# Optimization experiments

Hardware: AMD Instinct MI355X
Metric: run time of the kernel (lower is better)

The kernel has to match this reference:

```python
import jax, jax.numpy as jnp
import numpy as np

VOCAB = 100000
EMBED = 64
HIDDEN = 256
SEQ = 200
BATCH = 4096


def setup_inputs() -> dict:
    key = jax.random.key(0)
    ks = jax.random.split(key, 12)
    s = 0.02
    return {
        "user_hist": jax.random.randint(ks[0], (BATCH, SEQ), 0, VOCAB),
        "target_item": jax.random.randint(ks[1], (BATCH,), 0, VOCAB),
        "user_emb": jax.random.normal(ks[2], (VOCAB, EMBED), jnp.float32) * s,
        "item_emb": jax.random.normal(ks[3], (VOCAB, EMBED), jnp.float32) * s,
        "attn_w1": jax.random.normal(ks[4], (4 * EMBED, HIDDEN), jnp.float32) * s,
        "attn_b1": jnp.zeros((HIDDEN,), jnp.float32),
        "attn_w2": jax.random.normal(ks[5], (HIDDEN, 1), jnp.float32) * s,
        "attn_b2": jnp.zeros((1,), jnp.float32),
        "mlp_w1": jax.random.normal(ks[6], (2 * EMBED, HIDDEN), jnp.float32) * s,
        "mlp_b1": jnp.zeros((HIDDEN,), jnp.float32),
        "mlp_w2": jax.random.normal(ks[7], (HIDDEN, 1), jnp.float32) * s,
        "mlp_b2": jnp.zeros((1,), jnp.float32),
    }


def reference(user_hist, target_item, user_emb, item_emb,
              attn_w1, attn_b1, attn_w2, attn_b2,
              mlp_w1, mlp_b1, mlp_w2, mlp_b2):
    # [B, S, E] history embeddings, [B, 1, E] target embedding
    h = user_emb[user_hist]
    t = item_emb[target_item][:, None, :]
    tb = jnp.broadcast_to(t, h.shape)
    # attention MLP over [B, S, 4E]
    att_in = jnp.concatenate([h, tb, h - t, h * t], axis=-1)
    att_h = jax.nn.relu(att_in @ attn_w1 + attn_b1)
    att_logits = (att_h @ attn_w2 + attn_b2)[..., 0]            # [B, S]
    att_w = jax.nn.softmax(att_logits, axis=-1)[..., None]      # [B, S, 1]
    user_interest = jnp.sum(h * att_w, axis=1)                  # [B, E]
    # prediction head on [B, 2E]
    mlp_in = jnp.concatenate([user_interest, t[:, 0, :]], axis=-1)
    mlp_h = jax.nn.relu(mlp_in @ mlp_w1 + mlp_b1)
    out = jax.nn.sigmoid(mlp_h @ mlp_w2 + mlp_b2)               # [B, 1]
    return out
```

## Files before the change

### kernel.cpp

```cpp
#include <hip/hip_runtime.h>
#include <math.h>

#define EMBED   64
#define HIDDEN  256
#define SEQ     200
#define SEQP    208
#define MT      13

typedef _Float16 f16x8  __attribute__((ext_vector_type(8)));
typedef _Float16 half2_t __attribute__((ext_vector_type(2)));
typedef float    f32x4  __attribute__((ext_vector_type(4)));
typedef float    f32x2  __attribute__((ext_vector_type(2)));

__device__ inline float fdot2(half2_t a, half2_t b, float c) {
  return __builtin_amdgcn_fdot2(a, b, c, false);
}

__global__ void din_precompute(const float* __restrict__ attn_w1,
                               const float* __restrict__ mlp_w1,
                               uint2* __restrict__ fragB8,
                               _Float16* __restrict__ fragW3,
                               _Float16* __restrict__ D2f,
                               _Float16* __restrict__ fragB2) {
  const int gid = blockIdx.x * 256 + threadIdx.x;
  if (gid < 2048) {
    const int i = gid >> 7, rem = gid & 127, kc = rem >> 6, lane = rem & 63;
    const int n = i * 16 + (lane & 15);
    const int kb = kc * 32 + (lane >> 4) * 8;
    float v[8];
    #pragma unroll
    for (int j = 0; j < 8; ++j)
      v[j] = 16.0f * (attn_w1[(kb + j) * HIDDEN + n] + attn_w1[(128 + kb + j) * HIDDEN + n]);
    int lo = __builtin_amdgcn_cvt_pk_fp8_f32(v[0], v[1], 0, false);
    lo     = __builtin_amdgcn_cvt_pk_fp8_f32(v[2], v[3], lo, true);
    int hi = __builtin_amdgcn_cvt_pk_fp8_f32(v[4], v[5], 0, false);
    hi     = __builtin_amdgcn_cvt_pk_fp8_f32(v[6], v[7], hi, true);
    fragB8[gid] = uint2{(unsigned)lo, (unsigned)hi};
  } else if (gid < 4096) {
    const int g = gid - 2048;
    const int i = g >> 7, rem = g & 127, kc = rem >> 6, lane = rem & 63;
    const int n = i * 16 + (lane & 15);
    const int kb = kc * 32 + (lane >> 4) * 8;
    #pragma unroll
    for (int j = 0; j < 8; ++j)
      fragW3[g * 8 + j] = (_Float16)(16.0f * attn_w1[(192 + kb + j) * HIDDEN + n]);
  } else if (gid < 8192) {
    const int f = (gid - 4096) * 4;
    #pragma unroll
    for (int i = 0; i < 4; ++i) {
      const int idx = f + i;
      const int kk = idx & 7, t2 = idx >> 3;
      const int j = t2 & 255, c = t2 >> 8;
      const int k = c * 8 + kk;
      D2f[idx] = (_Float16)(attn_w1[(64 + k) * HIDDEN + j] - attn_w1[(128 + k) * HIDDEN + j]);
    }
  } else {
    const int g = gid - 8192;
    const int nt = g >> 8, kc = (g >> 6) & 3, lane = g & 63;
    const int n = nt * 16 + (lane & 15);
    const int kb = kc * 32 + (lane >> 4) * 8;
    #pragma unroll
    for (int j = 0; j < 8; ++j)
      fragB2[g * 8 + j] = (_Float16)mlp_w1[(kb + j) * HIDDEN + n];
  }
}

__global__ __launch_bounds__(512, 8)
void din_fused_kernel(const int* __restrict__ user_hist,
                      const int* __restrict__ target_item,
                      const float* __restrict__ user_emb,
                      const float* __restrict__ item_emb,
                      const float* __restrict__ attn_b1,
                      const float* __restrict__ attn_w2,
                      const float* __restrict__ mlp_b1,
                      const float* __restrict__ mlp_w2,
                      const float* __restrict__ mlp_b2,
                      const uint2* __restrict__ fragB8,
                      const _Float16* __restrict__ fragW3,
                      const _Float16* __restrict__ D2f,
                      const _Float16* __restrict__ fragB2,
                      float* __restrict__ out)
{
  __shared__ __align__(16) uint2 Hf8[MT * 2 * 64];
  __shared__ __align__(16) _Float16 t16[EMBED];
  __shared__ float cl[HIDDEN];
  __shared__ float lp[8][SEQP];
  __shared__ float weights[SEQP];
  __shared__ __align__(16) _Float16 mi16[EMBED];
  __shared__ float red[16];

  const int b    = blockIdx.x;
  const int tid  = threadIdx.x;
  const int lane = tid & 63;
  const int wave = tid >> 6;
  const int m    = lane & 15;
  const int quad = lane >> 4;

  if (tid < EMBED) t16[tid] = (_Float16)item_emb[target_item[b] * EMBED + tid];

  long long Aw8[2][2];
  #pragma unroll
  for (int i = 0; i < 2; ++i)
    #pragma unroll
    for (int c = 0; c < 2; ++c)
      Aw8[i][c] = __builtin_bit_cast(long long, fragB8[((2 * wave + i) * 2 + c) * 64 + lane]);

  {
    const int* hist = user_hist + b * SEQ;
    for (int slot = tid; slot < MT * 2 * 64; slot += 512) {
      const int ln = slot & 63, kcomb = slot >> 6;
      const int st = kcomb >> 1, kc = kcomb & 1;
      const int s = st * 16 + (ln & 15);
      const int kb = kc * 32 + (ln >> 4) * 8;
      uint2 pv = uint2{0u, 0u};
      if (s < SEQ) {
        const float4* src = reinterpret_cast<const float4*>(&user_emb[hist[s] * EMBED + kb]);
        const float4 x = src[0], y = src[1];
        int lo = __builtin_amdgcn_cvt_pk_fp8_f32(16.f * x.x, 16.f * x.y, 0, false);
        lo     = __builtin_amdgcn_cvt_pk_fp8_f32(16.f * x.z, 16.f * x.w, lo, true);
        int hi = __builtin_amdgcn_cvt_pk_fp8_f32(16.f * y.x, 16.f * y.y, 0, false);
        hi     = __builtin_amdgcn_cvt_pk_fp8_f32(16.f * y.z, 16.f * y.w, hi, true);
        pv = uint2{(unsigned)lo, (unsigned)hi};
      }
      Hf8[slot] = pv;
    }
  }
  __syncthreads();

  if (tid < HIDDEN) {
    float cj = attn_b1[tid];
    const f16x8* dp = reinterpret_cast<const f16x8*>(D2f);
    #pragma unroll
    for (int c = 0; c < 8; ++c) {
      const f16x8 dv = dp[c * HIDDEN + tid];
      const f16x8 tv = *reinterpret_cast<const f16x8*>(&t16[c * 8]);
      const half2_t* d2 = reinterpret_cast<const half2_t*>(&dv);
      const half2_t* t2 = reinterpret_cast<const half2_t*>(&tv);
      cj = fdot2(d2[0], t2[0], cj);
      cj = fdot2(d2[1], t2[1], cj);
      cj = fdot2(d2[2], t2[2], cj);
      cj = fdot2(d2[3], t2[3], cj);
    }
    cl[tid] = cj;
  }

  long long AwT[2][2];
  #pragma unroll
  for (int i = 0; i < 2; ++i)
    #pragma unroll
    for (int c = 0; c < 2; ++c) {
      const f16x8 w3v = reinterpret_cast<const f16x8*>(fragW3)[((2 * wave + i) * 2 + c) * 64 + lane];
      const f16x8 tw  = *reinterpret_cast<const f16x8*>(&t16[c * 32 + quad * 8]);
      const f16x8 p = w3v * tw;
      int lo = __builtin_amdgcn_cvt_pk_fp8_f32((float)p[0], (float)p[1], 0, false);
      lo     = __builtin_amdgcn_cvt_pk_fp8_f32((float)p[2], (float)p[3], lo, true);
      int hi = __builtin_amdgcn_cvt_pk_fp8_f32((float)p[4], (float)p[5], 0, false);
      hi     = __builtin_amdgcn_cvt_pk_fp8_f32((float)p[6], (float)p[7], hi, true);
      AwT[i][c] = __builtin_bit_cast(long long, uint2{(unsigned)lo, (unsigned)hi});
    }
  __syncthreads();

  float cn[2][4], w2n[2][4];
  #pragma unroll
  for (int i = 0; i < 2; ++i)
    #pragma unroll
    for (int r = 0; r < 4; ++r) {
      const int n = (2 * wave + i) * 16 + quad * 4 + r;
      cn[i][r]  = 256.0f * cl[n];
      w2n[i][r] = attn_w2[n] * (1.0f / 256.0f);
    }

  for (int st = 0; st < MT; ++st) {
    const long long b0 = __builtin_bit_cast(long long, Hf8[(st * 2 + 0) * 64 + lane]);
    const long long b1 = __builtin_bit_cast(long long, Hf8[(st * 2 + 1) * 64 + lane]);
    float lg = 0.f;
    #pragma unroll
    for (int i = 0; i < 2; ++i) {
      f32x4 acc = {cn[i][0], cn[i][1], cn[i][2], cn[i][3]};
      acc = __builtin_amdgcn_mfma_f32_16x16x32_fp8_fp8(Aw8[i][0], b0, acc, 0, 0, 0);
      acc = __builtin_amdgcn_mfma_f32_16x16x32_fp8_fp8(Aw8[i][1], b1, acc, 0, 0, 0);
      acc = __builtin_amdgcn_mfma_f32_16x16x32_fp8_fp8(AwT[i][0], b0, acc, 0, 0, 0);
      acc = __builtin_amdgcn_mfma_f32_16x16x32_fp8_fp8(AwT[i][1], b1, acc, 0, 0, 0);
      #pragma unroll
      for (int r = 0; r < 4; ++r)
        lg += fmaxf(acc[r], 0.0f) * w2n[i][r];
    }
    lg += __shfl_xor(lg, 16, 64);
    lg += __shfl_xor(lg, 32, 64);
    if (lane < 16) lp[wave][st * 16 + lane] = lg;
  }
  __syncthreads();

  float v = -INFINITY;
  if (tid < SEQ)
    v = lp[0][tid] + lp[1][tid] + lp[2][tid] + lp[3][tid]
      + lp[4][tid] + lp[5][tid] + lp[6][tid] + lp[7][tid];
  float mx = v;
  #pragma unroll
  for (int off = 32; off; off >>= 1) mx = fmaxf(mx, __shfl_xor(mx, off, 64));
  if (lane == 0) red[wave] = mx;
  __syncthreads();
  mx = fmaxf(fmaxf(fmaxf(red[0], red[1]), fmaxf(red[2], red[3])),
             fmaxf(fmaxf(red[4], red[5]), fmaxf(red[6], red[7])));
  float e = (tid < SEQ) ? expf(v - mx) : 0.0f;
  float ssum = e;
  #pragma unroll
  for (int off = 32; off; off >>= 1) ssum += __shfl_xor(ssum, off, 64);
  if (lane == 0) red[8 + wave] = ssum;
  __syncthreads();
  const float tot = red[8] + red[9] + red[10] + red[11]
                  + red[12] + red[13] + red[14] + red[15];
  if (tid < SEQP) weights[tid] = (tid < SEQ) ? e / tot : 0.0f;
  __syncthreads();

  {
    const int kc = wave & 1, g = wave >> 1;
    float pk[8];
    #pragma unroll
    for (int j = 0; j < 8; ++j) pk[j] = 0.f;
    for (int st = g; st < MT; st += 4) {
      const float wt = weights[st * 16 + m];
      const uint2 hv = Hf8[(st * 2 + kc) * 64 + lane];
      const f32x2 f0 = __builtin_amdgcn_cvt_pk_f32_fp8((int)hv.x, false);
      const f32x2 f1 = __builtin_amdgcn_cvt_pk_f32_fp8((int)hv.x, true);
      const f32x2 f2 = __builtin_amdgcn_cvt_pk_f32_fp8((int)hv.y, false);
      const f32x2 f3 = __builtin_amdgcn_cvt_pk_f32_fp8((int)hv.y, true);
      pk[0] += wt * f0.x;  pk[1] += wt * f0.y;
      pk[2] += wt * f1.x;  pk[3] += wt * f1.y;
      pk[4] += wt * f2.x;  pk[5] += wt * f2.y;
      pk[6] += wt * f3.x;  pk[7] += wt * f3.y;
    }
    #pragma unroll
    for (int j = 0; j < 8; ++j) {
      float p = pk[j];
      p += __shfl_xor(p, 1, 64);
      p += __shfl_xor(p, 2, 64);
      p += __shfl_xor(p, 4, 64);
      p += __shfl_xor(p, 8, 64);
      pk[j] = p;
    }
    if (m == 0) {
      #pragma unroll
      for (int j = 0; j < 8; ++j)
        lp[g][kc * 32 + quad * 8 + j] = pk[j];
    }
  }
  __syncthreads();
  if (tid < EMBED)
    mi16[tid] = (_Float16)((lp[0][tid] + lp[1][tid] + lp[2][tid] + lp[3][tid]) * 0.0625f);
  __syncthreads();

  {
    const f16x8 mb0 = *reinterpret_cast<const f16x8*>(&mi16[quad * 8]);
    const f16x8 mb1 = *reinterpret_cast<const f16x8*>(&mi16[32 + quad * 8]);
    const f16x8 tv0 = *reinterpret_cast<const f16x8*>(&t16[quad * 8]);
    const f16x8 tv1 = *reinterpret_cast<const f16x8*>(&t16[32 + quad * 8]);
    float z = 0.f;
    #pragma unroll
    for (int i = 0; i < 2; ++i) {
      const f16x8* B2 = reinterpret_cast<const f16x8*>(fragB2) + ((2 * wave + i) * 4) * 64 + lane;
      float bb[4], ww[4];
      #pragma unroll
      for (int r = 0; r < 4; ++r) {
        const int n = (2 * wave + i) * 16 + quad * 4 + r;
        bb[r] = mlp_b1[n];
        ww[r] = mlp_w2[n];
      }
      f32x4 acc = {bb[0], bb[1], bb[2], bb[3]};
      acc = __builtin_amdgcn_mfma_f32_16x16x32_f16(B2[0],       mb0, acc, 0, 0, 0);
      acc = __builtin_amdgcn_mfma_f32_16x16x32_f16(B2[64],      mb1, acc, 0, 0, 0);
      acc = __builtin_amdgcn_mfma_f32_16x16x32_f16(B2[128],     tv0, acc, 0, 0, 0);
      acc = __builtin_amdgcn_mfma_f32_16x16x32_f16(B2[192],     tv1, acc, 0, 0, 0);
      #pragma unroll
      for (int r = 0; r < 4; ++r)
        z += fmaxf(acc[r], 0.0f) * ww[r];
    }
    z += __shfl_xor(z, 16, 64);
    z += __shfl_xor(z, 32, 64);
    if (lane == 0) red[wave] = z;
  }
  __syncthreads();
  if (tid == 0) {
    const float zz = red[0] + red[1] + red[2] + red[3]
                   + red[4] + red[5] + red[6] + red[7] + mlp_b2[0];
    out[b] = 1.0f / (1.0f + expf(-zz));
  }
}

extern "C" void kernel_launch(void* const* d_in, const int* in_sizes, int n_in,
                              void* d_out, int out_size, void* d_ws, size_t ws_size,
                              hipStream_t stream) {
  const int*   user_hist   = (const int*)  d_in[0];
  const int*   target_item = (const int*)  d_in[1];
  const float* user_emb    = (const float*)d_in[2];
  const float* item_emb    = (const float*)d_in[3];
  const float* attn_w1     = (const float*)d_in[4];
  const float* attn_b1     = (const float*)d_in[5];
  const float* attn_w2     = (const float*)d_in[6];
  const float* mlp_w1      = (const float*)d_in[8];
  const float* mlp_b1      = (const float*)d_in[9];
  const float* mlp_w2      = (const float*)d_in[10];
  const float* mlp_b2      = (const float*)d_in[11];
  float* out = (float*)d_out;

  uint2*    fragB8 = (uint2*)d_ws;
  _Float16* fragW3 = (_Float16*)((char*)d_ws + 16384);
  _Float16* D2f    = (_Float16*)((char*)d_ws + 49152);
  _Float16* fragB2 = (_Float16*)((char*)d_ws + 81920);

  din_precompute<<<48, 256, 0, stream>>>(attn_w1, mlp_w1, fragB8, fragW3, D2f, fragB2);

  const int batch = in_sizes[1];
  din_fused_kernel<<<batch, 512, 0, stream>>>(
      user_hist, target_item, user_emb, item_emb,
      attn_b1, attn_w2, mlp_b1, mlp_w2, mlp_b2,
      fragB8, fragW3, D2f, fragB2, out);
}
```

Before: 183.1 us.

## Compute per-hidden bias term with MFMA and trim softmax to four waves

Replaces the scalar fdot2 loop that built the target-dependent bias vector cl in shared memory with a per-wave f16 MFMA over MFMA-fragment-layout weights, dropping the cl buffer and one barrier. History indices are staged in shared memory before the gather, the softmax reduction runs only on the four waves that cover the sequence, and the weighted-sum loop is fully unrolled, with vectorized bias and weight loads. This reduces serial per-block prologue work and synchronization, but adds an extra barrier before the gather and changes the precompute layout.

New measurement: 180.3 us. About the same (-1.5%).

```diff
diff --git a/kernel.cpp b/kernel.cpp
--- a/kernel.cpp
+++ b/kernel.cpp
@@ -8,19 +8,14 @@
 #define MT      13
 
 typedef _Float16 f16x8  __attribute__((ext_vector_type(8)));
-typedef _Float16 half2_t __attribute__((ext_vector_type(2)));
 typedef float    f32x4  __attribute__((ext_vector_type(4)));
 typedef float    f32x2  __attribute__((ext_vector_type(2)));
-
-__device__ inline float fdot2(half2_t a, half2_t b, float c) {
-  return __builtin_amdgcn_fdot2(a, b, c, false);
-}
 
 __global__ void din_precompute(const float* __restrict__ attn_w1,
                                const float* __restrict__ mlp_w1,
                                uint2* __restrict__ fragB8,
                                _Float16* __restrict__ fragW3,
-                               _Float16* __restrict__ D2f,
+                               _Float16* __restrict__ fragDt,
                                _Float16* __restrict__ fragB2) {
   const int gid = blockIdx.x * 256 + threadIdx.x;
   if (gid < 2048) {
@@ -44,18 +39,17 @@
     #pragma unroll
     for (int j = 0; j < 8; ++j)
       fragW3[g * 8 + j] = (_Float16)(16.0f * attn_w1[(192 + kb + j) * HIDDEN + n]);
-  } else if (gid < 8192) {
-    const int f = (gid - 4096) * 4;
-    #pragma unroll
-    for (int i = 0; i < 4; ++i) {
-      const int idx = f + i;
-      const int kk = idx & 7, t2 = idx >> 3;
-      const int j = t2 & 255, c = t2 >> 8;
-      const int k = c * 8 + kk;
-      D2f[idx] = (_Float16)(attn_w1[(64 + k) * HIDDEN + j] - attn_w1[(128 + k) * HIDDEN + j]);
-    }
+  } else if (gid < 6144) {
+    const int g = gid - 4096;
+    const int i = g >> 7, rem = g & 127, kc = rem >> 6, lane = rem & 63;
+    const int n = i * 16 + (lane & 15);
+    const int kb = kc * 32 + (lane >> 4) * 8;
+    #pragma unroll
+    for (int j = 0; j < 8; ++j)
+      fragDt[g * 8 + j] = (_Float16)(attn_w1[(64 + kb + j) * HIDDEN + n]
+                                   - attn_w1[(128 + kb + j) * HIDDEN + n]);
   } else {
-    const int g = gid - 8192;
+    const int g = gid - 6144;
     const int nt = g >> 8, kc = (g >> 6) & 3, lane = g & 63;
     const int n = nt * 16 + (lane & 15);
     const int kb = kc * 32 + (lane >> 4) * 8;
@@ -77,13 +71,13 @@
                       const float* __restrict__ mlp_b2,
                       const uint2* __restrict__ fragB8,
                       const _Float16* __restrict__ fragW3,
-                      const _Float16* __restrict__ D2f,
+                      const _Float16* __restrict__ fragDt,
                       const _Float16* __restrict__ fragB2,
                       float* __restrict__ out)
 {
   __shared__ __align__(16) uint2 Hf8[MT * 2 * 64];
   __shared__ __align__(16) _Float16 t16[EMBED];
-  __shared__ float cl[HIDDEN];
+  __shared__ int   histL[SEQP];
   __shared__ float lp[8][SEQP];
   __shared__ float weights[SEQP];
   __shared__ __align__(16) _Float16 mi16[EMBED];
@@ -97,6 +91,7 @@
   const int quad = lane >> 4;
 
   if (tid < EMBED) t16[tid] = (_Float16)item_emb[target_item[b] * EMBED + tid];
+  if (tid < SEQP) histL[tid] = (tid < SEQ) ? user_hist[b * SEQ + tid] : 0;
 
   long long Aw8[2][2];
   #pragma unroll
@@ -104,72 +99,68 @@
     #pragma unroll
     for (int c = 0; c < 2; ++c)
       Aw8[i][c] = __builtin_bit_cast(long long, fragB8[((2 * wave + i) * 2 + c) * 64 + lane]);
-
-  {
-    const int* hist = user_hist + b * SEQ;
-    for (int slot = tid; slot < MT * 2 * 64; slot += 512) {
-      const int ln = slot & 63, kcomb = slot >> 6;
-      const int st = kcomb >> 1, kc = kcomb & 1;
-      const int s = st * 16 + (ln & 15);
-      const int kb = kc * 32 + (ln >> 4) * 8;
-      uint2 pv = uint2{0u, 0u};
-      if (s < SEQ) {
-        const float4* src = reinterpret_cast<const float4*>(&user_emb[hist[s] * EMBED + kb]);
-        const float4 x = src[0], y = src[1];
-        int lo = __builtin_amdgcn_cvt_pk_fp8_f32(16.f * x.x, 16.f * x.y, 0, false);
-        lo     = __builtin_amdgcn_cvt_pk_fp8_f32(16.f * x.z, 16.f * x.w, lo, true);
-        int hi = __builtin_amdgcn_cvt_pk_fp8_f32(16.f * y.x, 16.f * y.y, 0, false);
-        hi     = __builtin_amdgcn_cvt_pk_fp8_f32(16.f * y.z, 16.f * y.w, hi, true);
-        pv = uint2{(unsigned)lo, (unsigned)hi};
-      }
-      Hf8[slot] = pv;
-    }
-  }
-  __syncthreads();
-
-  if (tid < HIDDEN) {
-    float cj = attn_b1[tid];
-    const f16x8* dp = reinterpret_cast<const f16x8*>(D2f);
-    #pragma unroll
-    for (int c = 0; c < 8; ++c) {
-      const f16x8 dv = dp[c * HIDDEN + tid];
-      const f16x8 tv = *reinterpret_cast<const f16x8*>(&t16[c * 8]);
-      const half2_t* d2 = reinterpret_cast<const half2_t*>(&dv);
-      const half2_t* t2 = reinterpret_cast<const half2_t*>(&tv);
-      cj = fdot2(d2[0], t2[0], cj);
-      cj = fdot2(d2[1], t2[1], cj);
-      cj = fdot2(d2[2], t2[2], cj);
-      cj = fdot2(d2[3], t2[3], cj);
-    }
-    cl[tid] = cj;
-  }
+  __syncthreads();
+
+  for (int slot = tid; slot < MT * 2 * 64; slot += 512) {
+    const int ln = slot & 63, kcomb = slot >> 6;
+    const int st = kcomb >> 1, kc = kcomb & 1;
+    const int s = st * 16 + (ln & 15);
+    const int kb = kc * 32 + (ln >> 4) * 8;
+    uint2 pv = uint2{0u, 0u};
+    if (s < SEQ) {
+      const float4* src = reinterpret_cast<const float4*>(&user_emb[histL[s] * EMBED + kb]);
+      const float4 x = src[0], y = src[1];
+      int lo = __builtin_amdgcn_cvt_pk_fp8_f32(16.f * x.x, 16.f * x.y, 0, false);
+      lo     = __builtin_amdgcn_cvt_pk_fp8_f32(16.f * x.z, 16.f * x.w, lo, true);
+      int hi = __builtin_amdgcn_cvt_pk_fp8_f32(16.f * y.x, 16.f * y.y, 0, false);
+      hi     = __builtin_amdgcn_cvt_pk_fp8_f32(16.f * y.z, 16.f * y.w, hi, true);
+      pv = uint2{(unsigned)lo, (unsigned)hi};
+    }
+    Hf8[slot] = pv;
+  }
+  __syncthreads();
+
+  const f16x8 tv0 = *reinterpret_cast<const f16x8*>(&t16[quad * 8]);
+  const f16x8 tv1 = *reinterpret_cast<const f16x8*>(&t16[32 + quad * 8]);
 
   long long AwT[2][2];
   #pragma unroll
-  for (int i = 0; i < 2; ++i)
+  for (int i = 0; i < 2; ++i) {
     #pragma unroll
     for (int c = 0; c < 2; ++c) {
       const f16x8 w3v = reinterpret_cast<const f16x8*>(fragW3)[((2 * wave + i) * 2 + c) * 64 + lane];
-      const f16x8 tw  = *reinterpret_cast<const f16x8*>(&t16[c * 32 + quad * 8]);
-      const f16x8 p = w3v * tw;
+      const f16x8 p = w3v * (c ? tv1 : tv0);
       int lo = __builtin_amdgcn_cvt_pk_fp8_f32((float)p[0], (float)p[1], 0, false);
       lo     = __builtin_amdgcn_cvt_pk_fp8_f32((float)p[2], (float)p[3], lo, true);
       int hi = __builtin_amdgcn_cvt_pk_fp8_f32((float)p[4], (float)p[5], 0, false);
       hi     = __builtin_amdgcn_cvt_pk_fp8_f32((float)p[6], (float)p[7], hi, true);
       AwT[i][c] = __builtin_bit_cast(long long, uint2{(unsigned)lo, (unsigned)hi});
     }
-  __syncthreads();
+  }
 
   float cn[2][4], w2n[2][4];
   #pragma unroll
-  for (int i = 0; i < 2; ++i)
-    #pragma unroll
-    for (int r = 0; r < 4; ++r) {
-      const int n = (2 * wave + i) * 16 + quad * 4 + r;
-      cn[i][r]  = 256.0f * cl[n];
-      w2n[i][r] = attn_w2[n] * (1.0f / 256.0f);
-    }
-
+  for (int i = 0; i < 2; ++i) {
+    const int tile = 2 * wave + i;
+    const f16x8 d0 = reinterpret_cast<const f16x8*>(fragDt)[(tile * 2 + 0) * 64 + lane];
+    const f16x8 d1 = reinterpret_cast<const f16x8*>(fragDt)[(tile * 2 + 1) * 64 + lane];
+    f32x4 acc = {0.f, 0.f, 0.f, 0.f};
+    acc = __builtin_amdgcn_mfma_f32_16x16x32_f16(d0, tv0, acc, 0, 0, 0);
+    acc = __builtin_amdgcn_mfma_f32_16x16x32_f16(d1, tv1, acc, 0, 0, 0);
+    const int nb = tile * 16 + quad * 4;
+    const float4 b1v = *reinterpret_cast<const float4*>(&attn_b1[nb]);
+    const float4 w2v = *reinterpret_cast<const float4*>(&attn_w2[nb]);
+    cn[i][0] = 256.0f * (b1v.x + acc[0]);
+    cn[i][1] = 256.0f * (b1v.y + acc[1]);
+    cn[i][2] = 256.0f * (b1v.z + acc[2]);
+    cn[i][3] = 256.0f * (b1v.w + acc[3]);
+    w2n[i][0] = w2v.x * (1.0f / 256.0f);
+    w2n[i][1] = w2v.y * (1.0f / 256.0f);
+    w2n[i][2] = w2v.z * (1.0f / 256.0f);
+    w2n[i][3] = w2v.w * (1.0f / 256.0f);
+  }
+
+  #pragma unroll 4
   for (int st = 0; st < MT; ++st) {
     const long long b0 = __builtin_bit_cast(long long, Hf8[(st * 2 + 0) * 64 + lane]);
     const long long b1 = __builtin_bit_cast(long long, Hf8[(st * 2 + 1) * 64 + lane]);
@@ -191,26 +182,30 @@
   }
   __syncthreads();
 
-  float v = -INFINITY;
-  if (tid < SEQ)
-    v = lp[0][tid] + lp[1][tid] + lp[2][tid] + lp[3][tid]
-      + lp[4][tid] + lp[5][tid] + lp[6][tid] + lp[7][tid];
-  float mx = v;
-  #pragma unroll
-  for (int off = 32; off; off >>= 1) mx = fmaxf(mx, __shfl_xor(mx, off, 64));
-  if (lane == 0) red[wave] = mx;
-  __syncthreads();
-  mx = fmaxf(fmaxf(fmaxf(red[0], red[1]), fmaxf(red[2], red[3])),
-             fmaxf(fmaxf(red[4], red[5]), fmaxf(red[6], red[7])));
-  float e = (tid < SEQ) ? expf(v - mx) : 0.0f;
-  float ssum = e;
-  #pragma unroll
-  for (int off = 32; off; off >>= 1) ssum += __shfl_xor(ssum, off, 64);
-  if (lane == 0) red[8 + wave] = ssum;
-  __syncthreads();
-  const float tot = red[8] + red[9] + red[10] + red[11]
-                  + red[12] + red[13] + red[14] + red[15];
-  if (tid < SEQP) weights[tid] = (tid < SEQ) ? e / tot : 0.0f;
+  float v = -INFINITY, e = 0.0f;
+  if (wave < 4) {
+    if (tid < SEQ)
+      v = lp[0][tid] + lp[1][tid] + lp[2][tid] + lp[3][tid]
+        + lp[4][tid] + lp[5][tid] + lp[6][tid] + lp[7][tid];
+    float mx = v;
+    #pragma unroll
+    for (int off = 32; off; off >>= 1) mx = fmaxf(mx, __shfl_xor(mx, off, 64));
+    if (lane == 0) red[wave] = mx;
+  }
+  __syncthreads();
+  if (wave < 4) {
+    const float mx = fmaxf(fmaxf(red[0], red[1]), fmaxf(red[2], red[3]));
+    e = (tid < SEQ) ? expf(v - mx) : 0.0f;
+    float ssum = e;
+    #pragma unroll
+    for (int off = 32; off; off >>= 1) ssum += __shfl_xor(ssum, off, 64);
+    if (lane == 0) red[4 + wave] = ssum;
+  }
+  __syncthreads();
+  if (wave < 4) {
+    const float tot = red[4] + red[5] + red[6] + red[7];
+    if (tid < SEQP) weights[tid] = (tid < SEQ) ? e / tot : 0.0f;
+  }
   __syncthreads();
 
   {
@@ -218,17 +213,21 @@
     float pk[8];
     #pragma unroll
     for (int j = 0; j < 8; ++j) pk[j] = 0.f;
-    for (int st = g; st < MT; st += 4) {
-      const float wt = weights[st * 16 + m];
-      const uint2 hv = Hf8[(st * 2 + kc) * 64 + lane];
-      const f32x2 f0 = __builtin_amdgcn_cvt_pk_f32_fp8((int)hv.x, false);
-      const f32x2 f1 = __builtin_amdgcn_cvt_pk_f32_fp8((int)hv.x, true);
-      const f32x2 f2 = __builtin_amdgcn_cvt_pk_f32_fp8((int)hv.y, false);
-      const f32x2 f3 = __builtin_amdgcn_cvt_pk_f32_fp8((int)hv.y, true);
-      pk[0] += wt * f0.x;  pk[1] += wt * f0.y;
-      pk[2] += wt * f1.x;  pk[3] += wt * f1.y;
-      pk[4] += wt * f2.x;  pk[5] += wt * f2.y;
-      pk[6] += wt * f3.x;  pk[7] += wt * f3.y;
+    #pragma unroll
+    for (int st2 = 0; st2 < 4; ++st2) {
+      const int st = g + st2 * 4;
+      if (st < MT) {
+        const float wt = weights[st * 16 + m];
+        const uint2 hv = Hf8[(st * 2 + kc) * 64 + lane];
+        const f32x2 f0 = __builtin_amdgcn_cvt_pk_f32_fp8((int)hv.x, false);
+        const f32x2 f1 = __builtin_amdgcn_cvt_pk_f32_fp8((int)hv.x, true);
+        const f32x2 f2 = __builtin_amdgcn_cvt_pk_f32_fp8((int)hv.y, false);
+        const f32x2 f3 = __builtin_amdgcn_cvt_pk_f32_fp8((int)hv.y, true);
+        pk[0] += wt * f0.x;  pk[1] += wt * f0.y;
+        pk[2] += wt * f1.x;  pk[3] += wt * f1.y;
+        pk[4] += wt * f2.x;  pk[5] += wt * f2.y;
+        pk[6] += wt * f3.x;  pk[7] += wt * f3.y;
+      }
     }
     #pragma unroll
     for (int j = 0; j < 8; ++j) {
@@ -253,27 +252,22 @@
   {
     const f16x8 mb0 = *reinterpret_cast<const f16x8*>(&mi16[quad * 8]);
     const f16x8 mb1 = *reinterpret_cast<const f16x8*>(&mi16[32 + quad * 8]);
-    const f16x8 tv0 = *reinterpret_cast<const f16x8*>(&t16[quad * 8]);
-    const f16x8 tv1 = *reinterpret_cast<const f16x8*>(&t16[32 + quad * 8]);
     float z = 0.f;
     #pragma unroll
     for (int i = 0; i < 2; ++i) {
       const f16x8* B2 = reinterpret_cast<const f16x8*>(fragB2) + ((2 * wave + i) * 4) * 64 + lane;
-      float bb[4], ww[4];
-      #pragma unroll
-      for (int r = 0; r < 4; ++r) {
-        const int n = (2 * wave + i) * 16 + quad * 4 + r;
-        bb[r] = mlp_b1[n];
-        ww[r] = mlp_w2[n];
-      }
-      f32x4 acc = {bb[0], bb[1], bb[2], bb[3]};
-      acc = __builtin_amdgcn_mfma_f32_16x16x32_f16(B2[0],       mb0, acc, 0, 0, 0);
-      acc = __builtin_amdgcn_mfma_f32_16x16x32_f16(B2[64],      mb1, acc, 0, 0, 0);
-      acc = __builtin_amdgcn_mfma_f32_16x16x32_f16(B2[128],     tv0, acc, 0, 0, 0);
-      acc = __builtin_amdgcn_mfma_f32_16x16x32_f16(B2[192],     tv1, acc, 0, 0, 0);
-      #pragma unroll
-      for (int r = 0; r < 4; ++r)
-        z += fmaxf(acc[r], 0.0f) * ww[r];
+      const int nb = (2 * wave + i) * 16 + quad * 4;
+      const float4 bb = *reinterpret_cast<const float4*>(&mlp_b1[nb]);
+      const float4 ww = *reinterpret_cast<const float4*>(&mlp_w2[nb]);
+      f32x4 acc = {bb.x, bb.y, bb.z, bb.w};
+      acc = __builtin_amdgcn_mfma_f32_16x16x32_f16(B2[0],   mb0, acc, 0, 0, 0);
+      acc = __builtin_amdgcn_mfma_f32_16x16x32_f16(B2[64],  mb1, acc, 0, 0, 0);
+      acc = __builtin_amdgcn_mfma_f32_16x16x32_f16(B2[128], tv0, acc, 0, 0, 0);
+      acc = __builtin_amdgcn_mfma_f32_16x16x32_f16(B2[192], tv1, acc, 0, 0, 0);
+      z += fmaxf(acc[0], 0.0f) * ww.x;
+      z += fmaxf(acc[1], 0.0f) * ww.y;
+      z += fmaxf(acc[2], 0.0f) * ww.z;
+      z += fmaxf(acc[3], 0.0f) * ww.w;
     }
     z += __shfl_xor(z, 16, 64);
     z += __shfl_xor(z, 32, 64);
@@ -305,14 +299,14 @@
 
   uint2*    fragB8 = (uint2*)d_ws;
   _Float16* fragW3 = (_Float16*)((char*)d_ws + 16384);
-  _Float16* D2f    = (_Float16*)((char*)d_ws + 49152);
+  _Float16* fragDt = (_Float16*)((char*)d_ws + 49152);
   _Float16* fragB2 = (_Float16*)((char*)d_ws + 81920);
 
-  din_precompute<<<48, 256, 0, stream>>>(attn_w1, mlp_w1, fragB8, fragW3, D2f, fragB2);
+  din_precompute<<<40, 256, 0, stream>>>(attn_w1, mlp_w1, fragB8, fragW3, fragDt, fragB2);
 
   const int batch = in_sizes[1];
   din_fused_kernel<<<batch, 512, 0, stream>>>(
       user_hist, target_item, user_emb, item_emb,
       attn_b1, attn_w2, mlp_b1, mlp_w2, mlp_b2,
-      fragB8, fragW3, D2f, fragB2, out);
+      fragB8, fragW3, fragDt, fragB2, out);
 }
```
